# Performance work log

Hardware: AMD Instinct MI355X
Metric: run time of the kernel (lower is better)

The kernel has to match this reference:

```python
import jax, jax.numpy as jnp
import numpy as np

NU, NI, D, L = 100_000, 150_000, 64, 3
N = NU + NI
NNZ_A, NNZ_S = 2_000_000, 800_000


def _spmm(rows, cols, vals, X, n):
    # sparse [n, m] @ X[m, D] via gather + segment-sum (COO)
    return jax.ops.segment_sum(vals[:, None] * X[cols], rows, num_segments=n)


def _bilinear(x, c, W, b):
    # nn.Bilinear(D, D, 1) with second arg a single broadcast vector c: x_n^T W c + b
    return x @ (W @ c) + b[0]  # [Nu]


def setup_inputs() -> dict:
    key = jax.random.key(0)
    ks = jax.random.split(key, 20)
    f = jnp.float32
    inp = {
        "u1": jax.random.normal(ks[0], (NU, D), f) * 0.1,
        "u2": jax.random.normal(ks[1], (NU, D), f) * 0.1,
        "item_emb": jax.random.normal(ks[2], (NI, D), f) * 0.1,
        "Wi": jax.random.normal(ks[3], (D, D), f) * (1.0 / np.sqrt(D)),
        "Wc": jax.random.normal(ks[4], (D, D), f) * (1.0 / np.sqrt(D)),
        "Ws": jax.random.normal(ks[5], (D, 2 * D), f) * (1.0 / np.sqrt(2 * D)),
        "fk_W": jax.random.normal(ks[6], (D, D), f) * (1.0 / np.sqrt(D)),
        "fk_b": jax.random.normal(ks[7], (1,), f) * 0.01,
        "A_vals": jax.random.uniform(ks[8], (NNZ_A,), f) * 0.2,
        "A2_vals": jax.random.uniform(ks[9], (NNZ_A,), f) * 0.2,
        "S_vals": jax.random.uniform(ks[10], (NNZ_S,), f) * 0.2,
        "A_rows": jax.random.randint(ks[11], (NNZ_A,), 0, N, jnp.int32),
        "A_cols": jax.random.randint(ks[12], (NNZ_A,), 0, N, jnp.int32),
        "A2_rows": jax.random.randint(ks[13], (NNZ_A,), 0, N, jnp.int32),
        "A2_cols": jax.random.randint(ks[14], (NNZ_A,), 0, N, jnp.int32),
        "S_rows": jax.random.randint(ks[15], (NNZ_S,), 0, NU, jnp.int32),
        "S_cols": jax.random.randint(ks[16], (NNZ_S,), 0, NU, jnp.int32),
        "shuffle1": jax.random.permutation(ks[17], NU).astype(jnp.int32),
        "shuffle2": jax.random.permutation(ks[18], NU).astype(jnp.int32),
    }
    return inp


def reference(u1, u2, item_emb, Wi, Wc, Ws, fk_W, fk_b,
              A_vals, A2_vals, S_vals,
              A_rows, A_cols, A2_rows, A2_cols, S_rows, S_cols,
              shuffle1, shuffle2):
    # CLDS.computer, epoch >= 2000 branch. S1 = S2 = socialGraph2 in the source.
    users_emb0 = (u1 + u2) * 0.5
    all_emb = jnp.concatenate([users_emb0, item_emb])  # [N, D]
    u1_neg = u1[shuffle1]
    u2_neg = u2[shuffle2]
    embs = [all_emb]
    logits_true, logits_false = [], []
    for layer in range(L):
        rows, cols, vals = (A_rows, A_cols, A_vals) if layer == 0 else (A2_rows, A2_cols, A2_vals)
        agg = _spmm(rows, cols, vals, all_emb, N)          # [N, D]
        u_int, items_next = agg[:NU], agg[NU:]
        u_next = jnp.tanh(u_int @ Wi.T)                     # social_i + tanh
        all_emb = jnp.concatenate([u_next, items_next])
        u1_soc = jnp.tanh(_spmm(S_rows, S_cols, S_vals, u1, NU) @ Wc.T)
        u2_soc = jnp.tanh(_spmm(S_rows, S_cols, S_vals, u2, NU) @ Wc.T)
        u1_neg = jnp.tanh(_spmm(S_rows, S_cols, S_vals, u1_neg, NU) @ Wc.T)
        u2_neg = jnp.tanh(_spmm(S_rows, S_cols, S_vals, u2_neg, NU) @ Wc.T)
        c1 = jnp.mean(u1_soc, axis=0)
        c2 = jnp.mean(u2_soc, axis=0)
        sc1 = _bilinear(u2_soc, c1, fk_W, fk_b)
        sc2 = _bilinear(u1_soc, c2, fk_W, fk_b)
        sc3 = _bilinear(u2_neg, c1, fk_W, fk_b)
        sc4 = _bilinear(u1_neg, c2, fk_W, fk_b)
        logits_true.append(jnp.concatenate([sc1, sc2]))     # [2*NU]
        logits_false.append(jnp.concatenate([sc3, sc4]))
        u_comb = (u1_soc + u2_soc) * 0.5
        users = jnp.concatenate([u_next, u_comb], axis=1) @ Ws.T
        users = users / jnp.linalg.norm(users)              # global L2 norm, as in torch .norm(2)
        embs.append(jnp.concatenate([users, items_next]))
    final = jnp.mean(jnp.stack(embs, axis=1), axis=1)       # [N, D]
    # torch: stack([1,2Nu] x 2L, dim=2) -> [1,2Nu,2L] -> view(1,-1)
    logits = jnp.stack(logits_true + logits_false, axis=1).reshape(1, -1)
    return final[:NU], final[NU:], logits
```

## Files before the change

### kernel.cpp

```cpp
#include <hip/hip_runtime.h>

#define NU 100000
#define NI 150000
#define NTOT 250000
#define DD 64
#define NNZ_A 2000000
#define NNZ_S 800000
#define SCAN_CHUNK 2048
#define NBS 49
#define NBA 123
#define GBS 391
#define GBA 977

typedef unsigned int uint;
typedef unsigned short ushort;

#define LB __launch_bounds__(256, 4)
#define RFL(x) __builtin_amdgcn_readfirstlane(x)

__device__ __forceinline__ uint f2bf_bits(float x) {
  uint a = __float_as_uint(x);
  return (a + 0x7fffu + ((a >> 16) & 1u)) >> 16;
}
__device__ __forceinline__ ushort f2bf(float x) { return (ushort)f2bf_bits(x); }
__device__ __forceinline__ float bf2f(ushort h) { return __uint_as_float(((uint)h) << 16); }
__device__ __forceinline__ uint pack_bf16x2(float lo, float hi) {
  return f2bf_bits(lo) | (f2bf_bits(hi) << 16);
}
__device__ __forceinline__ float unpk_lo(uint p) { return __uint_as_float(p << 16); }
__device__ __forceinline__ float unpk_hi(uint p) { return __uint_as_float(p & 0xffff0000u); }

__device__ __forceinline__ float tanh_fast(float x) {
  float e = __expf(2.0f * x);
  return 1.0f - __fdividef(2.0f, e + 1.0f);
}

__device__ __forceinline__ void gemm64x2_b(float aA, float aB,
                                           const float* __restrict__ Wt,
                                           volatile float* __restrict__ ab, int lane,
                                           float& oA, float& oB) {
  asm volatile("s_waitcnt lgkmcnt(0)" ::: "memory");
  __builtin_amdgcn_sched_barrier(0);
  ab[lane] = aA;
  ab[64 + lane] = aB;
  asm volatile("s_waitcnt lgkmcnt(0)" ::: "memory");
  __builtin_amdgcn_sched_barrier(0);
  float sA = 0.f, sB = 0.f;
#pragma unroll 4
  for (int k0 = 0; k0 < 64; k0 += 4) {
    float4 a4 = *(const float4*)(const float*)(ab + k0);
    float4 b4 = *(const float4*)(const float*)(ab + 64 + k0);
#pragma unroll
    for (int u = 0; u < 4; ++u) {
      float wk = Wt[(k0 + u) * 65 + lane];
      sA = fmaf(((const float*)&a4)[u], wk, sA);
      sB = fmaf(((const float*)&b4)[u], wk, sB);
    }
  }
  oA = sA; oB = sB;
}

__device__ __forceinline__ void gemm64x4_b(float a0, float a1, float a2, float a3,
                                           const float* __restrict__ Wt,
                                           volatile float* __restrict__ ab, int lane,
                                           float& o0, float& o1, float& o2, float& o3) {
  asm volatile("s_waitcnt lgkmcnt(0)" ::: "memory");
  __builtin_amdgcn_sched_barrier(0);
  ab[lane] = a0;
  ab[64 + lane] = a1;
  ab[128 + lane] = a2;
  ab[192 + lane] = a3;
  asm volatile("s_waitcnt lgkmcnt(0)" ::: "memory");
  __builtin_amdgcn_sched_barrier(0);
  float s0 = 0.f, s1 = 0.f, s2 = 0.f, s3 = 0.f;
#pragma unroll 4
  for (int k0 = 0; k0 < 64; k0 += 4) {
    float4 x0 = *(const float4*)(const float*)(ab + k0);
    float4 x1 = *(const float4*)(const float*)(ab + 64 + k0);
    float4 x2 = *(const float4*)(const float*)(ab + 128 + k0);
    float4 x3 = *(const float4*)(const float*)(ab + 192 + k0);
#pragma unroll
    for (int u = 0; u < 4; ++u) {
      float wk = Wt[(k0 + u) * 65 + lane];
      s0 = fmaf(((const float*)&x0)[u], wk, s0);
      s1 = fmaf(((const float*)&x1)[u], wk, s1);
      s2 = fmaf(((const float*)&x2)[u], wk, s2);
      s3 = fmaf(((const float*)&x3)[u], wk, s3);
    }
  }
  o0 = s0; o1 = s1; o2 = s2; o3 = s3;
}

__device__ __forceinline__ float gemm64x1_b(float a, const float* __restrict__ Wt,
                                            volatile float* __restrict__ ab, int lane) {
  asm volatile("s_waitcnt lgkmcnt(0)" ::: "memory");
  __builtin_amdgcn_sched_barrier(0);
  ab[lane] = a;
  asm volatile("s_waitcnt lgkmcnt(0)" ::: "memory");
  __builtin_amdgcn_sched_barrier(0);
  float s = 0.f;
#pragma unroll 4
  for (int k0 = 0; k0 < 64; k0 += 4) {
    float4 a4 = *(const float4*)(const float*)(ab + k0);
#pragma unroll
    for (int u = 0; u < 4; ++u)
      s = fmaf(((const float*)&a4)[u], Wt[(k0 + u) * 65 + lane], s);
  }
  return s;
}

__device__ __forceinline__ void stage_wt(const float* __restrict__ W, float* __restrict__ Wt) {
  for (int idx = threadIdx.x; idx < 64 * 64; idx += blockDim.x)
    Wt[(idx & 63) * 65 + (idx >> 6)] = W[idx];
  __syncthreads();
}

__global__ void k_init_items(const float* __restrict__ item, ushort* __restrict__ emb_bf,
                             float* __restrict__ out_final) {
  int idx = blockIdx.x * blockDim.x + threadIdx.x;
  const int tot = NI * DD;
  const int nu = NU * DD;
  for (; idx < tot; idx += gridDim.x * blockDim.x) {
    float v = item[idx];
    emb_bf[nu + idx] = f2bf(v);
    out_final[nu + idx] = 0.25f * v;
  }
}

__device__ __forceinline__ void hist_body(const int* rows, int* cnt, int* rank,
                                          int nnz, int bid, int nb) {
  int tid = bid * 256 + threadIdx.x;
  int gsz = nb * 256;
  for (int b = tid; b < nnz; b += gsz * 8) {
#pragma unroll
    for (int u = 0; u < 8; ++u) {
      int i = b + u * gsz;
      if (i < nnz) rank[i] = atomicAdd(&cnt[rows[i]], 1);
    }
  }
}

__global__ void k_hist3(const int* __restrict__ rowsS, int* __restrict__ cntS,
                        int* __restrict__ rankS,
                        const int* __restrict__ rowsA, int* __restrict__ cntA,
                        int* __restrict__ rankA,
                        const int* __restrict__ rowsA2, int* __restrict__ cntA2,
                        int* __restrict__ rankA2) {
  if ((int)blockIdx.x < GBS)
    hist_body(rowsS, cntS, rankS, NNZ_S, blockIdx.x, GBS);
  else if ((int)blockIdx.x < GBS + GBA)
    hist_body(rowsA, cntA, rankA, NNZ_A, blockIdx.x - GBS, GBA);
  else
    hist_body(rowsA2, cntA2, rankA2, NNZ_A, blockIdx.x - GBS - GBA, GBA);
}

__device__ __forceinline__ void scan1_body(const int* cnt, int* bsum, int n, int bid) {
  __shared__ int sdata[256];
  int base = bid * SCAN_CHUNK;
  int s = 0;
#pragma unroll
  for (int k = 0; k < 8; ++k) {
    int i = base + threadIdx.x * 8 + k;
    s += (i < n) ? cnt[i] : 0;
  }
  sdata[threadIdx.x] = s;
  __syncthreads();
  for (int off = 128; off > 0; off >>= 1) {
    if (threadIdx.x < off) sdata[threadIdx.x] += sdata[threadIdx.x + off];
    __syncthreads();
  }
  if (threadIdx.x == 0) bsum[bid] = sdata[0];
}

__global__ void k_scan1_3(const int* __restrict__ cntS, int* __restrict__ bsumS,
                          const int* __restrict__ cntA, int* __restrict__ bsumA,
                          const int* __restrict__ cntA2, int* __restrict__ bsumA2) {
  if ((int)blockIdx.x < NBS)            scan1_body(cntS, bsumS, NU, blockIdx.x);
  else if ((int)blockIdx.x < NBS + NBA) scan1_body(cntA, bsumA, NTOT, blockIdx.x - NBS);
  else                                  scan1_body(cntA2, bsumA2, NTOT, blockIdx.x - NBS - NBA);
}

__device__ __forceinline__ void scan2_body(int* bsum, int nb) {
  __shared__ int sdata[256];
  int v = (threadIdx.x < nb) ? bsum[threadIdx.x] : 0;
  sdata[threadIdx.x] = v;
  __syncthreads();
  for (int off = 1; off < 256; off <<= 1) {
    int t = (threadIdx.x >= (unsigned)off) ? sdata[threadIdx.x - off] : 0;
    __syncthreads();
    sdata[threadIdx.x] += t;
    __syncthreads();
  }
  if (threadIdx.x < nb) bsum[threadIdx.x] = sdata[threadIdx.x] - v;
}

__global__ void k_scan2_3(int* bsumS, int* bsumA, int* bsumA2) {
  if (blockIdx.x == 0)      scan2_body(bsumS, NBS);
  else if (blockIdx.x == 1) scan2_body(bsumA, NBA);
  else                      scan2_body(bsumA2, NBA);
}

__device__ __forceinline__ void scan3_body(const int* cnt, const int* bsum,
                                           int* rowptr, int n, int nnz, int bid) {
  __shared__ int sdata[256];
  int base = bid * SCAN_CHUNK;
  int loc[8];
  int s = 0;
#pragma unroll
  for (int k = 0; k < 8; ++k) {
    int i = base + threadIdx.x * 8 + k;
    loc[k] = (i < n) ? cnt[i] : 0;
    s += loc[k];
  }
  sdata[threadIdx.x] = s;
  __syncthreads();
  for (int off = 1; off < 256; off <<= 1) {
    int t = (threadIdx.x >= (unsigned)off) ? sdata[threadIdx.x - off] : 0;
    __syncthreads();
    sdata[threadIdx.x] += t;
    __syncthreads();
  }
  int pre = bsum[bid] + sdata[threadIdx.x] - s;
#pragma unroll
  for (int k = 0; k < 8; ++k) {
    int i = base + threadIdx.x * 8 + k;
    if (i < n) { rowptr[i] = pre; pre += loc[k]; }
  }
  if (bid == 0 && threadIdx.x == 0) rowptr[n] = nnz;
}

__global__ void k_scan3_3(const int* __restrict__ cntS, const int* __restrict__ bsumS,
                          int* __restrict__ ptrS,
                          const int* __restrict__ cntA, const int* __restrict__ bsumA,
                          int* __restrict__ ptrA,
                          const int* __restrict__ cntA2, const int* __restrict__ bsumA2,
                          int* __restrict__ ptrA2) {
  if ((int)blockIdx.x < NBS)            scan3_body(cntS, bsumS, ptrS, NU, NNZ_S, blockIdx.x);
  else if ((int)blockIdx.x < NBS + NBA) scan3_body(cntA, bsumA, ptrA, NTOT, NNZ_A, blockIdx.x - NBS);
  else                                  scan3_body(cntA2, bsumA2, ptrA2, NTOT, NNZ_A, blockIdx.x - NBS - NBA);
}

__device__ __forceinline__ void scatter_body(const int* rows, const int* cols,
                                             const float* vals, const int* ptr,
                                             const int* rank, int2* cv, int nnz,
                                             int bid, int nb) {
  int tid = bid * 256 + threadIdx.x;
  int gsz = nb * 256;
  for (int b = tid; b < nnz; b += gsz * 8) {
#pragma unroll
    for (int u = 0; u < 8; ++u) {
      int i = b + u * gsz;
      if (i < nnz) {
        int r = rows[i];
        cv[ptr[r] + rank[i]] = make_int2(cols[i], __float_as_int(vals[i]));
      }
    }
  }
  if (bid == 0 && threadIdx.x < 8) cv[nnz + threadIdx.x] = make_int2(0, 0);
}

__global__ void k_scatter1(const int* __restrict__ rows, const int* __restrict__ cols,
                           const float* __restrict__ vals, const int* __restrict__ ptr,
                           const int* __restrict__ rank, int2* __restrict__ cv, int nnz) {
  scatter_body(rows, cols, vals, ptr, rank, cv, nnz, blockIdx.x, gridDim.x);
}

__global__ void k_scatter2_2(const int* __restrict__ rowsS, const int* __restrict__ colsS,
                             const float* __restrict__ valsS, const int* __restrict__ ptrS,
                             const int* __restrict__ rankS, int2* __restrict__ cvS,
                             const int* __restrict__ rowsA, const int* __restrict__ colsA,
                             const float* __restrict__ valsA, const int* __restrict__ ptrA,
                             const int* __restrict__ rankA, int2* __restrict__ cvA) {
  if ((int)blockIdx.x < GBS)
    scatter_body(rowsS, colsS, valsS, ptrS, rankS, cvS, NNZ_S, blockIdx.x, GBS);
  else
    scatter_body(rowsA, colsA, valsA, ptrA, rankA, cvA, NNZ_A, blockIdx.x - GBS, GBA);
}

__global__ LB void k_transform(const float* __restrict__ u1, const float* __restrict__ u2,
                               const float* __restrict__ Wc, uint* __restrict__ SOCPt,
                               ushort* __restrict__ emb_bf, float* __restrict__ out_final) {
  __shared__ float Wt[64 * 65];
  __shared__ float AB[4][128];
  stage_wt(Wc, Wt);
  int lane = threadIdx.x & 63;
  volatile float* ab = AB[threadIdx.x >> 6];
  int wid = (blockIdx.x * blockDim.x + threadIdx.x) >> 6;
  int nw = (gridDim.x * blockDim.x) >> 6;
  for (int i = wid; i < NU; i += nw) {
    float a1 = u1[(size_t)i * DD + lane];
    float a2 = u2[(size_t)i * DD + lane];
    float v = 0.5f * (a1 + a2);
    emb_bf[(size_t)i * DD + lane] = f2bf(v);
    out_final[(size_t)i * DD + lane] = 0.25f * v;
    float o1, o2;
    gemm64x2_b(a1, a2, Wt, ab, lane, o1, o2);
    SOCPt[(size_t)i * DD + lane] = pack_bf16x2(o1, o2);
  }
}

__global__ void k_negmap(const uint* __restrict__ SOCPt, const int* __restrict__ s1,
                         const int* __restrict__ s2, uint2* __restrict__ QUADP) {
  int idx = blockIdx.x * blockDim.x + threadIdx.x;
  const int tot = NU * DD;
  for (; idx < tot; idx += gridDim.x * blockDim.x) {
    int i = idx >> 6, j = idx & 63;
    uint soc = SOCPt[idx];
    uint lo = SOCPt[(size_t)s1[i] * DD + j];
    uint hi = SOCPt[(size_t)s2[i] * DD + j];
    QUADP[idx] = make_uint2(soc, (lo & 0xffffu) | (hi & 0xffff0000u));
  }
}

__global__ LB void k_quadS(const int* __restrict__ rowptr, const int2* __restrict__ cv,
                           const uint2* __restrict__ QUADP, const float* __restrict__ Wc,
                           ushort* __restrict__ u1s, ushort* __restrict__ u2s,
                           ushort* __restrict__ n1o, ushort* __restrict__ n2o,
                           uint* __restrict__ NEGPa) {
  __shared__ float Wt[64 * 65];
  __shared__ float AB[4][128];
  stage_wt(Wc, Wt);
  int lane = threadIdx.x & 63;
  volatile float* ab = AB[threadIdx.x >> 6];
  int wid = (blockIdx.x * blockDim.x + threadIdx.x) >> 6;
  int nw = (gridDim.x * blockDim.x) >> 6;
  for (int r = wid; r < NU; r += nw) {
    int start = RFL(rowptr[r]);
    int n = RFL(rowptr[r + 1]) - start;
    float a1 = 0.f, a2 = 0.f, a3 = 0.f, a4 = 0.f;
    for (int k = 0; k < n; k += 8) {
      int2 e[8];
#pragma unroll
      for (int u = 0; u < 8; ++u) e[u] = cv[start + k + u];
      uint2 q[8];
#pragma unroll
      for (int u = 0; u < 8; ++u)
        q[u] = QUADP[(size_t)(uint)e[u].x * 64u + (uint)lane];
#pragma unroll
      for (int u = 0; u < 8; ++u) {
        float sv = (k + u < n) ? __int_as_float(e[u].y) : 0.f;
        a1 = fmaf(sv, unpk_lo(q[u].x), a1);
        a2 = fmaf(sv, unpk_hi(q[u].x), a2);
        a3 = fmaf(sv, unpk_lo(q[u].y), a3);
        a4 = fmaf(sv, unpk_hi(q[u].y), a4);
      }
    }
    float t1 = tanh_fast(a1), t2 = tanh_fast(a2), t3 = tanh_fast(a3), t4 = tanh_fast(a4);
    u1s[(size_t)r * DD + lane] = f2bf(t1);
    u2s[(size_t)r * DD + lane] = f2bf(t2);
    n1o[(size_t)r * DD + lane] = f2bf(t3);
    n2o[(size_t)r * DD + lane] = f2bf(t4);
    float o3, o4;
    gemm64x2_b(t3, t4, Wt, ab, lane, o3, o4);
    NEGPa[(size_t)r * DD + lane] = pack_bf16x2(o3, o4);
  }
}

__global__ LB void k_dualS(const int* __restrict__ rowptr, const int2* __restrict__ cv,
                           const uint* __restrict__ T, const float* __restrict__ Wc,
                           const float* __restrict__ wva, const float* __restrict__ wvb,
                           const float* __restrict__ fkb, float* __restrict__ out_logits,
                           int slot, uint* __restrict__ Tnext) {
  __shared__ float Wt[64 * 65];
  __shared__ float AB[4][256];
  stage_wt(Wc, Wt);
  int lane = threadIdx.x & 63;
  volatile float* ab = AB[threadIdx.x >> 6];
  int wid = (blockIdx.x * blockDim.x + threadIdx.x) >> 6;
  int nw = (gridDim.x * blockDim.x) >> 6;
  float b = fkb[0];
  float wa = wva[lane], wb = wvb[lane];
  for (int r = wid * 2; r < NU; r += nw * 2) {
    int s0 = RFL(rowptr[r]);
    int sm = RFL(rowptr[r + 1]);
    int s1e = RFL(rowptr[r + 2]);
    int n0 = sm - s0, n1 = s1e - sm;
    int kmax = max(n0, n1);
    float a0A = 0.f, a0B = 0.f, a1A = 0.f, a1B = 0.f;
    for (int k = 0; k < kmax; k += 8) {
      int b0 = (k < n0) ? s0 + k : s0;
      int b1 = (k < n1) ? sm + k : sm;
      int2 e0[8], e1[8];
#pragma unroll
      for (int u = 0; u < 8; ++u) e0[u] = cv[b0 + u];
#pragma unroll
      for (int u = 0; u < 8; ++u) e1[u] = cv[b1 + u];
      uint q0[8], q1[8];
#pragma unroll
      for (int u = 0; u < 8; ++u)
        q0[u] = T[(size_t)(uint)e0[u].x * 64u + (uint)lane];
#pragma unroll
      for (int u = 0; u < 8; ++u)
        q1[u] = T[(size_t)(uint)e1[u].x * 64u + (uint)lane];
#pragma unroll
      for (int u = 0; u < 8; ++u) {
        float sv0 = (k + u < n0) ? __int_as_float(e0[u].y) : 0.f;
        float sv1 = (k + u < n1) ? __int_as_float(e1[u].y) : 0.f;
        a0A = fmaf(sv0, unpk_lo(q0[u]), a0A);
        a0B = fmaf(sv0, unpk_hi(q0[u]), a0B);
        a1A = fmaf(sv1, unpk_lo(q1[u]), a1A);
        a1B = fmaf(sv1, unpk_hi(q1[u]), a1B);
      }
    }
    float t0a = tanh_fast(a0A), t0b = tanh_fast(a0B);
    float t1a = tanh_fast(a1A), t1b = tanh_fast(a1B);
    float p0a = t0a * wa, p0b = t0b * wb, p1a = t1a * wa, p1b = t1b * wb;
#pragma unroll
    for (int off = 32; off > 0; off >>= 1) {
      p0a += __shfl_xor(p0a, off);
      p0b += __shfl_xor(p0b, off);
      p1a += __shfl_xor(p1a, off);
      p1b += __shfl_xor(p1b, off);
    }
    if (lane == 0) {
      out_logits[(size_t)(NU + r) * 6 + slot] = p0a + b;
      out_logits[(size_t)r * 6 + slot] = p0b + b;
      out_logits[(size_t)(NU + r + 1) * 6 + slot] = p1a + b;
      out_logits[(size_t)(r + 1) * 6 + slot] = p1b + b;
    }
    if (Tnext) {
      float o0a, o0b, o1a, o1b;
      gemm64x4_b(t0a, t0b, t1a, t1b, Wt, ab, lane, o0a, o0b, o1a, o1b);
      Tnext[(size_t)r * DD + lane] = pack_bf16x2(o0a, o0b);
      Tnext[(size_t)(r + 1) * DD + lane] = pack_bf16x2(o1a, o1b);
    }
  }
}

__global__ LB void k_spmm_fusedA2(const int* __restrict__ rowptr, const int2* __restrict__ cv,
                                  const ushort* __restrict__ X, const float* __restrict__ W,
                                  ushort* __restrict__ embNext, float* __restrict__ outF) {
  __shared__ float Wt[64 * 65];
  __shared__ float AB[4][256];
  stage_wt(W, Wt);
  int lane = threadIdx.x & 63;
  volatile float* ab = AB[threadIdx.x >> 6];
  int wid = (blockIdx.x * blockDim.x + threadIdx.x) >> 6;
  int nw = (gridDim.x * blockDim.x) >> 6;
  for (int r = wid * 4; r < NTOT; r += nw * 4) {
    int sp[5];
#pragma unroll
    for (int i = 0; i < 5; ++i) sp[i] = RFL(rowptr[r + i]);
    int n0 = sp[1] - sp[0], n1 = sp[2] - sp[1];
    int n2 = sp[3] - sp[2], n3 = sp[4] - sp[3];
    int kmax = max(max(n0, n1), max(n2, n3));
    float acc0 = 0.f, acc1 = 0.f, acc2 = 0.f, acc3 = 0.f;
    for (int k = 0; k < kmax; k += 8) {
      int b0 = (k < n0) ? sp[0] + k : sp[0];
      int b1 = (k < n1) ? sp[1] + k : sp[1];
      int b2 = (k < n2) ? sp[2] + k : sp[2];
      int b3 = (k < n3) ? sp[3] + k : sp[3];
      int2 e0[8], e1[8], e2[8], e3[8];
#pragma unroll
      for (int u = 0; u < 8; ++u) e0[u] = cv[b0 + u];
#pragma unroll
      for (int u = 0; u < 8; ++u) e1[u] = cv[b1 + u];
#pragma unroll
      for (int u = 0; u < 8; ++u) e2[u] = cv[b2 + u];
#pragma unroll
      for (int u = 0; u < 8; ++u) e3[u] = cv[b3 + u];
      uint h0[8], h1[8], h2[8], h3[8];
#pragma unroll
      for (int u = 0; u < 8; ++u)
        h0[u] = X[(size_t)(uint)e0[u].x * 64u + (uint)lane];
#pragma unroll
      for (int u = 0; u < 8; ++u)
        h1[u] = X[(size_t)(uint)e1[u].x * 64u + (uint)lane];
#pragma unroll
      for (int u = 0; u < 8; ++u)
        h2[u] = X[(size_t)(uint)e2[u].x * 64u + (uint)lane];
#pragma unroll
      for (int u = 0; u < 8; ++u)
        h3[u] = X[(size_t)(uint)e3[u].x * 64u + (uint)lane];
#pragma unroll
      for (int u = 0; u < 8; ++u) {
        float sv0 = (k + u < n0) ? __int_as_float(e0[u].y) : 0.f;
        float sv1 = (k + u < n1) ? __int_as_float(e1[u].y) : 0.f;
        float sv2 = (k + u < n2) ? __int_as_float(e2[u].y) : 0.f;
        float sv3 = (k + u < n3) ? __int_as_float(e3[u].y) : 0.f;
        acc0 = fmaf(sv0, __uint_as_float(h0[u] << 16), acc0);
        acc1 = fmaf(sv1, __uint_as_float(h1[u] << 16), acc1);
        acc2 = fmaf(sv2, __uint_as_float(h2[u] << 16), acc2);
        acc3 = fmaf(sv3, __uint_as_float(h3[u] << 16), acc3);
      }
    }
    if (r < NU) {
      float o0, o1, o2, o3;
      gemm64x4_b(acc0, acc1, acc2, acc3, Wt, ab, lane, o0, o1, o2, o3);
      embNext[(size_t)r * DD + lane] = f2bf(tanh_fast(o0));
      embNext[(size_t)(r + 1) * DD + lane] = f2bf(tanh_fast(o1));
      embNext[(size_t)(r + 2) * DD + lane] = f2bf(tanh_fast(o2));
      embNext[(size_t)(r + 3) * DD + lane] = f2bf(tanh_fast(o3));
    } else {
      embNext[(size_t)r * DD + lane] = f2bf(acc0);
      embNext[(size_t)(r + 1) * DD + lane] = f2bf(acc1);
      embNext[(size_t)(r + 2) * DD + lane] = f2bf(acc2);
      embNext[(size_t)(r + 3) * DD + lane] = f2bf(acc3);
      outF[(size_t)r * DD + lane] += 0.25f * acc0;
      outF[(size_t)(r + 1) * DD + lane] += 0.25f * acc1;
      outF[(size_t)(r + 2) * DD + lane] += 0.25f * acc2;
      outF[(size_t)(r + 3) * DD + lane] += 0.25f * acc3;
    }
  }
}

__global__ void k_colsum2(const ushort* __restrict__ x1, const ushort* __restrict__ x2,
                          float* __restrict__ c1, float* __restrict__ c2) {
  int lane = threadIdx.x & 63;
  int wid = (blockIdx.x * blockDim.x + threadIdx.x) >> 6;
  int nw = (gridDim.x * blockDim.x) >> 6;
  float a1 = 0.f, a2 = 0.f;
  for (int i = wid; i < NU; i += nw) {
    a1 += bf2f(x1[(size_t)i * DD + lane]);
    a2 += bf2f(x2[(size_t)i * DD + lane]);
  }
  atomicAdd(&c1[lane], a1);
  atomicAdd(&c2[lane], a2);
}

__global__ void k_wvec(const float* __restrict__ fkW, const float* __restrict__ c1r,
                       const float* __restrict__ c2r, float* __restrict__ w1,
                       float* __restrict__ w2) {
  int j = threadIdx.x;
  float a1 = 0.f, a2 = 0.f;
  for (int k = 0; k < 64; ++k) {
    float w = fkW[j * 64 + k];
    a1 += w * c1r[k];
    a2 += w * c2r[k];
  }
  w1[j] = a1 * (1.0f / NU);
  w2[j] = a2 * (1.0f / NU);
}

__global__ void k_logits4(const ushort* __restrict__ u1s, const ushort* __restrict__ u2s,
                          const ushort* __restrict__ n1o, const ushort* __restrict__ n2o,
                          const float* __restrict__ w1, const float* __restrict__ w2,
                          const float* __restrict__ fkb, float* __restrict__ out_logits) {
  int lane = threadIdx.x & 63;
  int wid = (blockIdx.x * blockDim.x + threadIdx.x) >> 6;
  int nw = (gridDim.x * blockDim.x) >> 6;
  float b = fkb[0];
  for (int i = wid; i < 2 * NU; i += nw) {
    bool lo = i < NU;
    int r = lo ? i : i - NU;
    const ushort* xs = lo ? u2s : u1s;
    const ushort* xn = lo ? n2o : n1o;
    const float* wv = lo ? w1 : w2;
    float wvl = wv[lane];
    float ps = bf2f(xs[(size_t)r * DD + lane]) * wvl;
    float pn = bf2f(xn[(size_t)r * DD + lane]) * wvl;
#pragma unroll
    for (int off = 32; off > 0; off >>= 1) {
      ps += __shfl_xor(ps, off);
      pn += __shfl_xor(pn, off);
    }
    if (lane == 0) {
      float vs = ps + b;
      out_logits[(size_t)i * 6 + 0] = vs;
      out_logits[(size_t)i * 6 + 1] = vs;
      out_logits[(size_t)i * 6 + 2] = vs;
      out_logits[(size_t)i * 6 + 3] = pn + b;
    }
  }
}

__global__ LB void k_comb_gemm(const ushort* __restrict__ u1s, const ushort* __restrict__ u2s,
                               const float* __restrict__ Ws, ushort* __restrict__ UC) {
  __shared__ float Wt[64 * 65];
  __shared__ float AB[4][128];
  for (int idx = threadIdx.x; idx < 64 * 64; idx += blockDim.x)
    Wt[(idx & 63) * 65 + (idx >> 6)] = Ws[(idx >> 6) * 128 + 64 + (idx & 63)];
  __syncthreads();
  int lane = threadIdx.x & 63;
  volatile float* ab = AB[threadIdx.x >> 6];
  int wid = (blockIdx.x * blockDim.x + threadIdx.x) >> 6;
  int nw = (gridDim.x * blockDim.x) >> 6;
  for (int i = wid; i < NU; i += nw) {
    float c = 0.5f * (bf2f(u1s[(size_t)i * DD + lane]) + bf2f(u2s[(size_t)i * DD + lane]));
    UC[(size_t)i * DD + lane] = f2bf(gemm64x1_b(c, Wt, ab, lane));
  }
}

__global__ LB void k_users(const ushort* __restrict__ u_next, const ushort* __restrict__ uc,
                           const float* __restrict__ Ws, float* __restrict__ users_raw,
                           float* __restrict__ sumsq) {
  __shared__ float Wt[64 * 65];
  __shared__ float AB[4][128];
  for (int idx = threadIdx.x; idx < 64 * 64; idx += blockDim.x)
    Wt[(idx & 63) * 65 + (idx >> 6)] = Ws[(idx >> 6) * 128 + (idx & 63)];
  __syncthreads();
  int lane = threadIdx.x & 63;
  volatile float* ab = AB[threadIdx.x >> 6];
  int wid = (blockIdx.x * blockDim.x + threadIdx.x) >> 6;
  int nw = (gridDim.x * blockDim.x) >> 6;
  float ss = 0.f;
  for (int i = wid; i < NU; i += nw) {
    float va = bf2f(u_next[(size_t)i * DD + lane]);
    float acc = bf2f(uc[(size_t)i * DD + lane]) + gemm64x1_b(va, Wt, ab, lane);
    users_raw[(size_t)i * DD + lane] = acc;
    ss += acc * acc;
  }
#pragma unroll
  for (int off = 32; off > 0; off >>= 1) ss += __shfl_xor(ss, off);
  if (lane == 0) atomicAdd(sumsq, ss);
}

__global__ void k_users_acc(const float* __restrict__ users_raw,
                            const float* __restrict__ sumsq, float* __restrict__ out_final) {
  float scale = 0.25f / sqrtf(*sumsq);
  int idx = blockIdx.x * blockDim.x + threadIdx.x;
  for (; idx < NU * DD; idx += gridDim.x * blockDim.x)
    out_final[idx] += users_raw[idx] * scale;
}

extern "C" void kernel_launch(void* const* d_in, const int* in_sizes, int n_in,
                              void* d_out, int out_size, void* d_ws, size_t ws_size,
                              hipStream_t stream) {
  const float* u1      = (const float*)d_in[0];
  const float* u2      = (const float*)d_in[1];
  const float* item    = (const float*)d_in[2];
  const float* Wi      = (const float*)d_in[3];
  const float* Wc      = (const float*)d_in[4];
  const float* Ws      = (const float*)d_in[5];
  const float* fk_W    = (const float*)d_in[6];
  const float* fk_b    = (const float*)d_in[7];
  const float* A_vals  = (const float*)d_in[8];
  const float* A2_vals = (const float*)d_in[9];
  const float* S_vals  = (const float*)d_in[10];
  const int*   A_rows  = (const int*)d_in[11];
  const int*   A_cols  = (const int*)d_in[12];
  const int*   A2_rows = (const int*)d_in[13];
  const int*   A2_cols = (const int*)d_in[14];
  const int*   S_rows  = (const int*)d_in[15];
  const int*   S_cols  = (const int*)d_in[16];
  const int*   sh1     = (const int*)d_in[17];
  const int*   sh2     = (const int*)d_in[18];

  float* ws = (float*)d_ws;
  ushort* embA_bf = (ushort*)ws;
  ushort* embB_bf = (ushort*)(ws + 8000000);
  uint2*  QUADP   = (uint2*)(ws + 16000000);
  int*    rankS2  = (int*)(ws + 16000000);
  int*    rankA   = (int*)(ws + 16800000);
  int*    cntS    = (int*)(ws + 18800000);
  int*    cntA    = (int*)(ws + 18900000);
  int*    bsumS   = (int*)(ws + 19150000);
  int*    bsumA   = (int*)(ws + 19150256);
  int*    bsumA2  = (int*)(ws + 19150512);
  uint*   NEGPb   = (uint*)(ws + 16000000);
  float*  uraw    = ws + 22400000;
  uint*   NEGPa   = (uint*)(ws + 28800000);
  ushort* u1s     = (ushort*)(ws + 35200000);
  ushort* u2s     = (ushort*)(ws + 38400000);
  int2*   cvA2    = (int2*)(ws + 35200000);
  uint*   SOCPt   = (uint*)(ws + 41600000);
  ushort* n1o     = (ushort*)(ws + 41600000);
  ushort* UCb     = (ushort*)(ws + 41600000);
  ushort* n2o     = (ushort*)(ws + 44800000);
  int2*   cvA     = (int2*)(ws + 48000000);
  int2*   cvS     = (int2*)(ws + 52000016);
  int*    ptrA    = (int*)(ws + 53600032);
  int*    ptrS    = ptrA + (NTOT + 1);
  int*    cntA2   = ptrS + (NU + 1);
  int*    bsum_un = cntA2 + NTOT;
  float*  c1r     = (float*)(bsum_un + 256);
  float*  c2r     = c1r + 64;
  float*  w1      = c2r + 64;
  float*  w2      = w1 + 64;
  float*  sumsq   = w2 + 64;
  int*    rankA2  = (int*)(ws + 54200580);
  int*    ptrA2   = (int*)(ws + 56200580);

  float* out        = (float*)d_out;
  float* out_logits = out + (size_t)NTOT * DD;

  hipMemsetAsync(cntS, 0, 350000 * sizeof(int), stream);
  hipMemsetAsync(cntA2, 0, (size_t)NTOT * sizeof(int), stream);
  k_hist3<<<GBS + 2 * GBA, 256, 0, stream>>>(S_rows, cntS, rankS2,
                                             A_rows, cntA, rankA,
                                             A2_rows, cntA2, rankA2);
  k_scan1_3<<<NBS + 2 * NBA, 256, 0, stream>>>(cntS, bsumS, cntA, bsumA, cntA2, bsumA2);
  k_scan2_3<<<3, 256, 0, stream>>>(bsumS, bsumA, bsumA2);
  k_scan3_3<<<NBS + 2 * NBA, 256, 0, stream>>>(cntS, bsumS, ptrS,
                                               cntA, bsumA, ptrA,
                                               cntA2, bsumA2, ptrA2);
  k_scatter2_2<<<GBS + GBA, 256, 0, stream>>>(S_rows, S_cols, S_vals, ptrS, rankS2, cvS,
                                              A_rows, A_cols, A_vals, ptrA, rankA, cvA);

  hipMemsetAsync(c1r, 0, 128 * sizeof(float), stream);
  k_init_items<<<1024, 256, 0, stream>>>(item, embA_bf, out);
  k_transform<<<1024, 256, 0, stream>>>(u1, u2, Wc, SOCPt, embA_bf, out);
  k_negmap<<<1024, 256, 0, stream>>>(SOCPt, sh1, sh2, QUADP);

  k_quadS<<<2048, 256, 0, stream>>>(ptrS, cvS, QUADP, Wc, u1s, u2s, n1o, n2o, NEGPa);
  k_colsum2<<<256, 256, 0, stream>>>(u1s, u2s, c1r, c2r);
  k_wvec<<<1, 64, 0, stream>>>(fk_W, c1r, c2r, w1, w2);
  k_logits4<<<1024, 256, 0, stream>>>(u1s, u2s, n1o, n2o, w1, w2, fk_b, out_logits);
  k_comb_gemm<<<1024, 256, 0, stream>>>(u1s, u2s, Ws, UCb);

  k_scatter1<<<GBA, 256, 0, stream>>>(A2_rows, A2_cols, A2_vals, ptrA2, rankA2,
                                      cvA2, NNZ_A);

  ushort* embCur = embA_bf;
  ushort* embNext = embB_bf;
  for (int l = 0; l < 3; ++l) {
    const int* pA = (l == 0) ? ptrA : ptrA2;
    const int2* cA = (l == 0) ? cvA : cvA2;

    k_spmm_fusedA2<<<4096, 256, 0, stream>>>(pA, cA, embCur, Wi, embNext, out);

    if (l == 1)
      k_dualS<<<2048, 256, 0, stream>>>(ptrS, cvS, NEGPa, Wc, w2, w1, fk_b,
                                        out_logits, 4, NEGPb);
    else if (l == 2)
      k_dualS<<<2048, 256, 0, stream>>>(ptrS, cvS, NEGPb, Wc, w2, w1, fk_b,
                                        out_logits, 5, (uint*)nullptr);

    hipMemsetAsync(sumsq, 0, sizeof(float), stream);
    k_users<<<1024, 256, 0, stream>>>(embNext, UCb, Ws, uraw, sumsq);
    k_users_acc<<<2048, 256, 0, stream>>>(uraw, sumsq, out);

    { ushort* t = embCur; embCur = embNext; embNext = t; }
  }
}
```

Before: 1.458 ms.

## Merge independent kernels into block-range-dispatched megakernels

Combines histogram, user transform and item init into one launch, fuses logits and comb gemm into one launch, and runs the A2 scatter alongside the layer-0 SpMM. The layer loop is unrolled on the host. The aim is to cut launch overhead and idle tails between small independent kernels by letting them share one grid. The risk is that merged kernels carry larger shared memory and launch bounds, which may lower occupancy for the lighter branches.

```diff
diff --git a/kernel.cpp b/kernel.cpp
--- a/kernel.cpp
+++ b/kernel.cpp
@@ -11,6 +11,9 @@
 #define NBA 123
 #define GBS 391
 #define GBA 977
+#define HB (GBS + 2 * GBA)
+#define TB 1024
+#define IB 512
 
 typedef unsigned int uint;
 typedef unsigned short ushort;
@@ -115,18 +118,6 @@
   __syncthreads();
 }
 
-__global__ void k_init_items(const float* __restrict__ item, ushort* __restrict__ emb_bf,
-                             float* __restrict__ out_final) {
-  int idx = blockIdx.x * blockDim.x + threadIdx.x;
-  const int tot = NI * DD;
-  const int nu = NU * DD;
-  for (; idx < tot; idx += gridDim.x * blockDim.x) {
-    float v = item[idx];
-    emb_bf[nu + idx] = f2bf(v);
-    out_final[nu + idx] = 0.25f * v;
-  }
-}
-
 __device__ __forceinline__ void hist_body(const int* rows, int* cnt, int* rank,
                                           int nnz, int bid, int nb) {
   int tid = bid * 256 + threadIdx.x;
@@ -140,18 +131,70 @@
   }
 }
 
-__global__ void k_hist3(const int* __restrict__ rowsS, int* __restrict__ cntS,
-                        int* __restrict__ rankS,
-                        const int* __restrict__ rowsA, int* __restrict__ cntA,
-                        int* __restrict__ rankA,
-                        const int* __restrict__ rowsA2, int* __restrict__ cntA2,
-                        int* __restrict__ rankA2) {
-  if ((int)blockIdx.x < GBS)
-    hist_body(rowsS, cntS, rankS, NNZ_S, blockIdx.x, GBS);
-  else if ((int)blockIdx.x < GBS + GBA)
-    hist_body(rowsA, cntA, rankA, NNZ_A, blockIdx.x - GBS, GBA);
-  else
-    hist_body(rowsA2, cntA2, rankA2, NNZ_A, blockIdx.x - GBS - GBA, GBA);
+__device__ __forceinline__ void scatter_body(const int* rows, const int* cols,
+                                             const float* vals, const int* ptr,
+                                             const int* rank, int2* cv, int nnz,
+                                             int bid, int nb) {
+  int tid = bid * 256 + threadIdx.x;
+  int gsz = nb * 256;
+  for (int b = tid; b < nnz; b += gsz * 8) {
+#pragma unroll
+    for (int u = 0; u < 8; ++u) {
+      int i = b + u * gsz;
+      if (i < nnz) {
+        int r = rows[i];
+        cv[ptr[r] + rank[i]] = make_int2(cols[i], __float_as_int(vals[i]));
+      }
+    }
+  }
+  if (bid == 0 && threadIdx.x < 8) cv[nnz + threadIdx.x] = make_int2(0, 0);
+}
+
+__global__ LB void k_mega1(const int* __restrict__ rowsS, int* __restrict__ cntS,
+                           int* __restrict__ rankS,
+                           const int* __restrict__ rowsA, int* __restrict__ cntA,
+                           int* __restrict__ rankA,
+                           const int* __restrict__ rowsA2, int* __restrict__ cntA2,
+                           int* __restrict__ rankA2,
+                           const float* __restrict__ u1, const float* __restrict__ u2,
+                           const float* __restrict__ Wc, uint* __restrict__ SOCPt,
+                           const float* __restrict__ item,
+                           ushort* __restrict__ emb_bf, float* __restrict__ out_final) {
+  __shared__ float Wt[64 * 65];
+  __shared__ float AB[4][128];
+  int bid = blockIdx.x;
+  if (bid < GBS) {
+    hist_body(rowsS, cntS, rankS, NNZ_S, bid, GBS);
+  } else if (bid < GBS + GBA) {
+    hist_body(rowsA, cntA, rankA, NNZ_A, bid - GBS, GBA);
+  } else if (bid < HB) {
+    hist_body(rowsA2, cntA2, rankA2, NNZ_A, bid - GBS - GBA, GBA);
+  } else if (bid < HB + TB) {
+    stage_wt(Wc, Wt);
+    int lane = threadIdx.x & 63;
+    volatile float* ab = AB[threadIdx.x >> 6];
+    int wid = ((bid - HB) * 256 + (int)threadIdx.x) >> 6;
+    int nw = (TB * 256) >> 6;
+    for (int i = wid; i < NU; i += nw) {
+      float a1 = u1[(size_t)i * DD + lane];
+      float a2 = u2[(size_t)i * DD + lane];
+      float v = 0.5f * (a1 + a2);
+      emb_bf[(size_t)i * DD + lane] = f2bf(v);
+      out_final[(size_t)i * DD + lane] = 0.25f * v;
+      float o1, o2;
+      gemm64x2_b(a1, a2, Wt, ab, lane, o1, o2);
+      SOCPt[(size_t)i * DD + lane] = pack_bf16x2(o1, o2);
+    }
+  } else {
+    int idx = (bid - HB - TB) * 256 + threadIdx.x;
+    const int tot = NI * DD;
+    const int nu = NU * DD;
+    for (; idx < tot; idx += IB * 256) {
+      float v = item[idx];
+      emb_bf[nu + idx] = f2bf(v);
+      out_final[nu + idx] = 0.25f * v;
+    }
+  }
 }
 
 __device__ __forceinline__ void scan1_body(const int* cnt, int* bsum, int n, int bid) {
@@ -240,31 +283,6 @@
   else                                  scan3_body(cntA2, bsumA2, ptrA2, NTOT, NNZ_A, blockIdx.x - NBS - NBA);
 }
 
-__device__ __forceinline__ void scatter_body(const int* rows, const int* cols,
-                                             const float* vals, const int* ptr,
-                                             const int* rank, int2* cv, int nnz,
-                                             int bid, int nb) {
-  int tid = bid * 256 + threadIdx.x;
-  int gsz = nb * 256;
-  for (int b = tid; b < nnz; b += gsz * 8) {
-#pragma unroll
-    for (int u = 0; u < 8; ++u) {
-      int i = b + u * gsz;
-      if (i < nnz) {
-        int r = rows[i];
-        cv[ptr[r] + rank[i]] = make_int2(cols[i], __float_as_int(vals[i]));
-      }
-    }
-  }
-  if (bid == 0 && threadIdx.x < 8) cv[nnz + threadIdx.x] = make_int2(0, 0);
-}
-
-__global__ void k_scatter1(const int* __restrict__ rows, const int* __restrict__ cols,
-                           const float* __restrict__ vals, const int* __restrict__ ptr,
-                           const int* __restrict__ rank, int2* __restrict__ cv, int nnz) {
-  scatter_body(rows, cols, vals, ptr, rank, cv, nnz, blockIdx.x, gridDim.x);
-}
-
 __global__ void k_scatter2_2(const int* __restrict__ rowsS, const int* __restrict__ colsS,
                              const float* __restrict__ valsS, const int* __restrict__ ptrS,
                              const int* __restrict__ rankS, int2* __restrict__ cvS,
@@ -275,28 +293,6 @@
     scatter_body(rowsS, colsS, valsS, ptrS, rankS, cvS, NNZ_S, blockIdx.x, GBS);
   else
     scatter_body(rowsA, colsA, valsA, ptrA, rankA, cvA, NNZ_A, blockIdx.x - GBS, GBA);
-}
-
-__global__ LB void k_transform(const float* __restrict__ u1, const float* __restrict__ u2,
-                               const float* __restrict__ Wc, uint* __restrict__ SOCPt,
-                               ushort* __restrict__ emb_bf, float* __restrict__ out_final) {
-  __shared__ float Wt[64 * 65];
-  __shared__ float AB[4][128];
-  stage_wt(Wc, Wt);
-  int lane = threadIdx.x & 63;
-  volatile float* ab = AB[threadIdx.x >> 6];
-  int wid = (blockIdx.x * blockDim.x + threadIdx.x) >> 6;
-  int nw = (gridDim.x * blockDim.x) >> 6;
-  for (int i = wid; i < NU; i += nw) {
-    float a1 = u1[(size_t)i * DD + lane];
-    float a2 = u2[(size_t)i * DD + lane];
-    float v = 0.5f * (a1 + a2);
-    emb_bf[(size_t)i * DD + lane] = f2bf(v);
-    out_final[(size_t)i * DD + lane] = 0.25f * v;
-    float o1, o2;
-    gemm64x2_b(a1, a2, Wt, ab, lane, o1, o2);
-    SOCPt[(size_t)i * DD + lane] = pack_bf16x2(o1, o2);
-  }
 }
 
 __global__ void k_negmap(const uint* __restrict__ SOCPt, const int* __restrict__ s1,
@@ -427,16 +423,15 @@
   }
 }
 
-__global__ LB void k_spmm_fusedA2(const int* __restrict__ rowptr, const int2* __restrict__ cv,
-                                  const ushort* __restrict__ X, const float* __restrict__ W,
-                                  ushort* __restrict__ embNext, float* __restrict__ outF) {
-  __shared__ float Wt[64 * 65];
-  __shared__ float AB[4][256];
-  stage_wt(W, Wt);
+__device__ __forceinline__ void fusedA2_body(const int* __restrict__ rowptr,
+                                             const int2* __restrict__ cv,
+                                             const ushort* __restrict__ X,
+                                             float* __restrict__ Wt,
+                                             volatile float* __restrict__ ab,
+                                             ushort* __restrict__ embNext,
+                                             float* __restrict__ outF,
+                                             int wid, int nw) {
   int lane = threadIdx.x & 63;
-  volatile float* ab = AB[threadIdx.x >> 6];
-  int wid = (blockIdx.x * blockDim.x + threadIdx.x) >> 6;
-  int nw = (gridDim.x * blockDim.x) >> 6;
   for (int r = wid * 4; r < NTOT; r += nw * 4) {
     int sp[5];
 #pragma unroll
@@ -504,6 +499,35 @@
   }
 }
 
+__global__ LB void k_spmm_fusedA2(const int* __restrict__ rowptr, const int2* __restrict__ cv,
+                                  const ushort* __restrict__ X, const float* __restrict__ W,
+                                  ushort* __restrict__ embNext, float* __restrict__ outF) {
+  __shared__ float Wt[64 * 65];
+  __shared__ float AB[4][256];
+  stage_wt(W, Wt);
+  int wid = (blockIdx.x * blockDim.x + threadIdx.x) >> 6;
+  int nw = (gridDim.x * blockDim.x) >> 6;
+  fusedA2_body(rowptr, cv, X, Wt, AB[threadIdx.x >> 6], embNext, outF, wid, nw);
+}
+
+__global__ LB void k_l0(const int* __restrict__ rowsA2, const int* __restrict__ colsA2,
+                        const float* __restrict__ valsA2, const int* __restrict__ ptrA2,
+                        const int* __restrict__ rankA2, int2* __restrict__ cvA2,
+                        const int* __restrict__ rowptr, const int2* __restrict__ cv,
+                        const ushort* __restrict__ X, const float* __restrict__ W,
+                        ushort* __restrict__ embNext, float* __restrict__ outF) {
+  __shared__ float Wt[64 * 65];
+  __shared__ float AB[4][256];
+  if ((int)blockIdx.x < GBA) {
+    scatter_body(rowsA2, colsA2, valsA2, ptrA2, rankA2, cvA2, NNZ_A, blockIdx.x, GBA);
+  } else {
+    stage_wt(W, Wt);
+    int wid = (((int)blockIdx.x - GBA) * 256 + (int)threadIdx.x) >> 6;
+    int nw = (4096 * 256) >> 6;
+    fusedA2_body(rowptr, cv, X, Wt, AB[threadIdx.x >> 6], embNext, outF, wid, nw);
+  }
+}
+
 __global__ void k_colsum2(const ushort* __restrict__ x1, const ushort* __restrict__ x2,
                           float* __restrict__ c1, float* __restrict__ c2) {
   int lane = threadIdx.x & 63;
@@ -532,52 +556,51 @@
   w2[j] = a2 * (1.0f / NU);
 }
 
-__global__ void k_logits4(const ushort* __restrict__ u1s, const ushort* __restrict__ u2s,
+__global__ LB void k_post(const ushort* __restrict__ u1s, const ushort* __restrict__ u2s,
                           const ushort* __restrict__ n1o, const ushort* __restrict__ n2o,
                           const float* __restrict__ w1, const float* __restrict__ w2,
-                          const float* __restrict__ fkb, float* __restrict__ out_logits) {
-  int lane = threadIdx.x & 63;
-  int wid = (blockIdx.x * blockDim.x + threadIdx.x) >> 6;
-  int nw = (gridDim.x * blockDim.x) >> 6;
-  float b = fkb[0];
-  for (int i = wid; i < 2 * NU; i += nw) {
-    bool lo = i < NU;
-    int r = lo ? i : i - NU;
-    const ushort* xs = lo ? u2s : u1s;
-    const ushort* xn = lo ? n2o : n1o;
-    const float* wv = lo ? w1 : w2;
-    float wvl = wv[lane];
-    float ps = bf2f(xs[(size_t)r * DD + lane]) * wvl;
-    float pn = bf2f(xn[(size_t)r * DD + lane]) * wvl;
-#pragma unroll
-    for (int off = 32; off > 0; off >>= 1) {
-      ps += __shfl_xor(ps, off);
-      pn += __shfl_xor(pn, off);
-    }
-    if (lane == 0) {
-      float vs = ps + b;
-      out_logits[(size_t)i * 6 + 0] = vs;
-      out_logits[(size_t)i * 6 + 1] = vs;
-      out_logits[(size_t)i * 6 + 2] = vs;
-      out_logits[(size_t)i * 6 + 3] = pn + b;
-    }
-  }
-}
-
-__global__ LB void k_comb_gemm(const ushort* __restrict__ u1s, const ushort* __restrict__ u2s,
-                               const float* __restrict__ Ws, ushort* __restrict__ UC) {
+                          const float* __restrict__ fkb, float* __restrict__ out_logits,
+                          const float* __restrict__ Ws, ushort* __restrict__ UC) {
   __shared__ float Wt[64 * 65];
   __shared__ float AB[4][128];
-  for (int idx = threadIdx.x; idx < 64 * 64; idx += blockDim.x)
-    Wt[(idx & 63) * 65 + (idx >> 6)] = Ws[(idx >> 6) * 128 + 64 + (idx & 63)];
-  __syncthreads();
   int lane = threadIdx.x & 63;
-  volatile float* ab = AB[threadIdx.x >> 6];
-  int wid = (blockIdx.x * blockDim.x + threadIdx.x) >> 6;
-  int nw = (gridDim.x * blockDim.x) >> 6;
-  for (int i = wid; i < NU; i += nw) {
-    float c = 0.5f * (bf2f(u1s[(size_t)i * DD + lane]) + bf2f(u2s[(size_t)i * DD + lane]));
-    UC[(size_t)i * DD + lane] = f2bf(gemm64x1_b(c, Wt, ab, lane));
+  if ((int)blockIdx.x < 1024) {
+    int wid = (blockIdx.x * 256 + threadIdx.x) >> 6;
+    int nw = (1024 * 256) >> 6;
+    float b = fkb[0];
+    for (int i = wid; i < 2 * NU; i += nw) {
+      bool lo = i < NU;
+      int r = lo ? i : i - NU;
+      const ushort* xs = lo ? u2s : u1s;
+      const ushort* xn = lo ? n2o : n1o;
+      const float* wv = lo ? w1 : w2;
+      float wvl = wv[lane];
+      float ps = bf2f(xs[(size_t)r * DD + lane]) * wvl;
+      float pn = bf2f(xn[(size_t)r * DD + lane]) * wvl;
+#pragma unroll
+      for (int off = 32; off > 0; off >>= 1) {
+        ps += __shfl_xor(ps, off);
+        pn += __shfl_xor(pn, off);
+      }
+      if (lane == 0) {
+        float vs = ps + b;
+        out_logits[(size_t)i * 6 + 0] = vs;
+        out_logits[(size_t)i * 6 + 1] = vs;
+        out_logits[(size_t)i * 6 + 2] = vs;
+        out_logits[(size_t)i * 6 + 3] = pn + b;
+      }
+    }
+  } else {
+    for (int idx = threadIdx.x; idx < 64 * 64; idx += blockDim.x)
+      Wt[(idx & 63) * 65 + (idx >> 6)] = Ws[(idx >> 6) * 128 + 64 + (idx & 63)];
+    __syncthreads();
+    volatile float* ab = AB[threadIdx.x >> 6];
+    int wid = (((int)blockIdx.x - 1024) * 256 + (int)threadIdx.x) >> 6;
+    int nw = (1024 * 256) >> 6;
+    for (int i = wid; i < NU; i += nw) {
+      float c = 0.5f * (bf2f(u1s[(size_t)i * DD + lane]) + bf2f(u2s[(size_t)i * DD + lane]));
+      UC[(size_t)i * DD + lane] = f2bf(gemm64x1_b(c, Wt, ab, lane));
+    }
   }
 }
 
@@ -662,8 +685,8 @@
   int*    ptrA    = (int*)(ws + 53600032);
   int*    ptrS    = ptrA + (NTOT + 1);
   int*    cntA2   = ptrS + (NU + 1);
-  int*    bsum_un = cntA2 + NTOT;
-  float*  c1r     = (float*)(bsum_un + 256);
+  int*    spare   = cntA2 + NTOT;
+  float*  c1r     = (float*)(spare + 256);
   float*  c2r     = c1r + 64;
   float*  w1      = c2r + 64;
   float*  w2      = w1 + 64;
@@ -676,9 +699,12 @@
 
   hipMemsetAsync(cntS, 0, 350000 * sizeof(int), stream);
   hipMemsetAsync(cntA2, 0, (size_t)NTOT * sizeof(int), stream);
-  k_hist3<<<GBS + 2 * GBA, 256, 0, stream>>>(S_rows, cntS, rankS2,
-                                             A_rows, cntA, rankA,
-                                             A2_rows, cntA2, rankA2);
+  hipMemsetAsync(c1r, 0, 128 * sizeof(float), stream);
+  k_mega1<<<HB + TB + IB, 256, 0, stream>>>(S_rows, cntS, rankS2,
+                                            A_rows, cntA, rankA,
+                                            A2_rows, cntA2, rankA2,
+                                            u1, u2, Wc, SOCPt, item, embA_bf, out);
+
   k_scan1_3<<<NBS + 2 * NBA, 256, 0, stream>>>(cntS, bsumS, cntA, bsumA, cntA2, bsumA2);
   k_scan2_3<<<3, 256, 0, stream>>>(bsumS, bsumA, bsumA2);
   k_scan3_3<<<NBS + 2 * NBA, 256, 0, stream>>>(cntS, bsumS, ptrS,
@@ -687,39 +713,29 @@
   k_scatter2_2<<<GBS + GBA, 256, 0, stream>>>(S_rows, S_cols, S_vals, ptrS, rankS2, cvS,
                                               A_rows, A_cols, A_vals, ptrA, rankA, cvA);
 
-  hipMemsetAsync(c1r, 0, 128 * sizeof(float), stream);
-  k_init_items<<<1024, 256, 0, stream>>>(item, embA_bf, out);
-  k_transform<<<1024, 256, 0, stream>>>(u1, u2, Wc, SOCPt, embA_bf, out);
   k_negmap<<<1024, 256, 0, stream>>>(SOCPt, sh1, sh2, QUADP);
-
   k_quadS<<<2048, 256, 0, stream>>>(ptrS, cvS, QUADP, Wc, u1s, u2s, n1o, n2o, NEGPa);
   k_colsum2<<<256, 256, 0, stream>>>(u1s, u2s, c1r, c2r);
   k_wvec<<<1, 64, 0, stream>>>(fk_W, c1r, c2r, w1, w2);
-  k_logits4<<<1024, 256, 0, stream>>>(u1s, u2s, n1o, n2o, w1, w2, fk_b, out_logits);
-  k_comb_gemm<<<1024, 256, 0, stream>>>(u1s, u2s, Ws, UCb);
-
-  k_scatter1<<<GBA, 256, 0, stream>>>(A2_rows, A2_cols, A2_vals, ptrA2, rankA2,
-                                      cvA2, NNZ_A);
-
-  ushort* embCur = embA_bf;
-  ushort* embNext = embB_bf;
-  for (int l = 0; l < 3; ++l) {
-    const int* pA = (l == 0) ? ptrA : ptrA2;
-    const int2* cA = (l == 0) ? cvA : cvA2;
-
-    k_spmm_fusedA2<<<4096, 256, 0, stream>>>(pA, cA, embCur, Wi, embNext, out);
-
-    if (l == 1)
-      k_dualS<<<2048, 256, 0, stream>>>(ptrS, cvS, NEGPa, Wc, w2, w1, fk_b,
-                                        out_logits, 4, NEGPb);
-    else if (l == 2)
-      k_dualS<<<2048, 256, 0, stream>>>(ptrS, cvS, NEGPb, Wc, w2, w1, fk_b,
-                                        out_logits, 5, (uint*)nullptr);
-
-    hipMemsetAsync(sumsq, 0, sizeof(float), stream);
-    k_users<<<1024, 256, 0, stream>>>(embNext, UCb, Ws, uraw, sumsq);
-    k_users_acc<<<2048, 256, 0, stream>>>(uraw, sumsq, out);
-
-    { ushort* t = embCur; embCur = embNext; embNext = t; }
-  }
-}
+  k_post<<<2048, 256, 0, stream>>>(u1s, u2s, n1o, n2o, w1, w2, fk_b, out_logits, Ws, UCb);
+
+  k_l0<<<GBA + 4096, 256, 0, stream>>>(A2_rows, A2_cols, A2_vals, ptrA2, rankA2, cvA2,
+                                       ptrA, cvA, embA_bf, Wi, embB_bf, out);
+  hipMemsetAsync(sumsq, 0, sizeof(float), stream);
+  k_users<<<1024, 256, 0, stream>>>(embB_bf, UCb, Ws, uraw, sumsq);
+  k_users_acc<<<2048, 256, 0, stream>>>(uraw, sumsq, out);
+
+  k_spmm_fusedA2<<<4096, 256, 0, stream>>>(ptrA2, cvA2, embB_bf, Wi, embA_bf, out);
+  k_dualS<<<2048, 256, 0, stream>>>(ptrS, cvS, NEGPa, Wc, w2, w1, fk_b,
+                                    out_logits, 4, NEGPb);
+  hipMemsetAsync(sumsq, 0, sizeof(float), stream);
+  k_users<<<1024, 256, 0, stream>>>(embA_bf, UCb, Ws, uraw, sumsq);
+  k_users_acc<<<2048, 256, 0, stream>>>(uraw, sumsq, out);
+
+  k_spmm_fusedA2<<<4096, 256, 0, stream>>>(ptrA2, cvA2, embA_bf, Wi, embB_bf, out);
+  k_dualS<<<2048, 256, 0, stream>>>(ptrS, cvS, NEGPb, Wc, w2, w1, fk_b,
+                                    out_logits, 5, (uint*)nullptr);
+  hipMemsetAsync(sumsq, 0, sizeof(float), stream);
+  k_users<<<1024, 256, 0, stream>>>(embB_bf, UCb, Ws, uraw, sumsq);
+  k_users_acc<<<2048, 256, 0, stream>>>(uraw, sumsq, out);
+}
```

After: 1.444 ms. No clear change (-0.9%).
